# Optimization experiments

Measured on AMD Instinct MI355X. Metric: run time of the kernel, lower is better.

## Reference

```python
import jax, jax.numpy as jnp
import numpy as np

N = 12288          # neuron_count (nodes.shape[0])
R = 1024           # retina_output_size[1]
B = 32             # batch
N_LAYERS = 4       # CONNECTOME_LAYER_NUMBER
DENSITY = 0.05     # adjacency (connectome) sparsity
N_VISUAL = 2048    # neurons flagged 'visual'
N_RATIONAL = 64    # neurons flagged 'rational'


def setup_inputs() -> dict:
    key = jax.random.key(0)
    k_x, k_ret, k_sh, k_adj, k_rat, k_vis, k_ridx = jax.random.split(key, 7)

    x = jax.random.normal(k_x, (B, R), dtype=jnp.float32)

    # Retina layer: Linear(R -> N, bias=False); only rows at visual indices nonzero.
    vis_idx = jax.random.permutation(k_vis, N)[:N_VISUAL]
    vis_mask = jnp.zeros((N,), jnp.float32).at[vis_idx].set(1.0)
    W_retina = jax.random.normal(k_ret, (N, R), dtype=jnp.float32) * vis_mask[:, None]

    # Shared connectome weights: rand(N,N) masked by transposed adjacency != 0.
    adj = jax.random.bernoulli(k_adj, DENSITY, (N, N)).astype(jnp.float32)
    W_shared = jax.random.uniform(k_sh, (N, N), dtype=jnp.float32) * adj

    # Rational layer: Linear(N -> 2); only columns at rational indices nonzero.
    rat_idx = jax.random.permutation(k_ridx, N)[:N_RATIONAL]
    rat_mask = jnp.zeros((N,), jnp.float32).at[rat_idx].set(1.0)
    W_rational = jax.random.normal(k_rat, (2, N), dtype=jnp.float32) * rat_mask[None, :]

    return {"x": x, "W_retina": W_retina, "W_shared": W_shared,
            "W_rational": W_rational, "n_layers": N_LAYERS}


def reference(x, W_retina, W_shared, W_rational, n_layers):
    # retina: out = x @ W_retina^T   -> [B, N]
    out = jnp.einsum('br,nr->bn', x, W_retina)
    # repeated shared-weight Linear (bias-free): out = out @ W_shared^T
    for _ in range(n_layers):
        out = jnp.einsum('bn,mn->bm', out, W_shared)
    # rational readout: [B, 2]
    return jnp.einsum('bn,on->bo', out, W_rational)
```

## Files before the change

### kernel.cpp

```cpp
#include <hip/hip_runtime.h>
#include <cstddef>

#define NN 12288
#define RR 1024
#define BB 32

#define MSEGS 128
#define MROWS (NN / MSEGS)
#define JBLK (NN / 1024)
#define CAP 20

#define PSEGS 256
#define PJ (NN / PSEGS)

typedef float vfloat4 __attribute__((ext_vector_type(4)));

__global__ __launch_bounds__(256) void build_kernel(
    const float* __restrict__ W, float* __restrict__ sval,
    unsigned char* __restrict__ scnt)
{
    const int t   = threadIdx.x;
    const int jb  = blockIdx.x;
    const int seg = blockIdx.y;
    const int j   = jb * 1024 + t * 4;
    const int m0  = seg * MROWS;

    const vfloat4* Wp = (const vfloat4*)(W + (size_t)m0 * NN + j);
    float* v0 = sval + ((size_t)seg * NN + j) * CAP;
    float* v1 = v0 + CAP;
    float* v2 = v0 + 2 * CAP;
    float* v3 = v0 + 3 * CAP;

    int c0 = 0, c1 = 0, c2 = 0, c3 = 0;
    for (int i = 0; i < MROWS; i += 16) {
        vfloat4 w[16];
        #pragma unroll
        for (int u = 0; u < 16; ++u)
            w[u] = __builtin_nontemporal_load(Wp + (size_t)u * (NN / 4));
        Wp += 4 * NN;
        #pragma unroll
        for (int u = 0; u < 16; ++u) {
            const unsigned int li = (unsigned)(i + u);
            if (w[u].x != 0.f) { unsigned int b = __float_as_uint(w[u].x); if (c0 < CAP) v0[c0] = __uint_as_float((b & 0xFFFFFF00u) | li); c0++; }
            if (w[u].y != 0.f) { unsigned int b = __float_as_uint(w[u].y); if (c1 < CAP) v1[c1] = __uint_as_float((b & 0xFFFFFF00u) | li); c1++; }
            if (w[u].z != 0.f) { unsigned int b = __float_as_uint(w[u].z); if (c2 < CAP) v2[c2] = __uint_as_float((b & 0xFFFFFF00u) | li); c2++; }
            if (w[u].w != 0.f) { unsigned int b = __float_as_uint(w[u].w); if (c3 < CAP) v3[c3] = __uint_as_float((b & 0xFFFFFF00u) | li); c3++; }
        }
    }
    uchar4 cn;
    cn.x = (unsigned char)(c0 < CAP ? c0 : CAP);
    cn.y = (unsigned char)(c1 < CAP ? c1 : CAP);
    cn.z = (unsigned char)(c2 < CAP ? c2 : CAP);
    cn.w = (unsigned char)(c3 < CAP ? c3 : CAP);
    *(uchar4*)(scnt + (size_t)seg * NN + j) = cn;
}

__global__ __launch_bounds__(256) void sfold_kernel(
    const float* __restrict__ sval, const unsigned char* __restrict__ scnt,
    const float* __restrict__ hin, float* __restrict__ hpart)
{
    const int seg = blockIdx.y;
    const int j   = blockIdx.x * 256 + threadIdx.x;
    const int m0  = seg * MROWS;

    __shared__ float2 hs[MROWS];
    if (threadIdx.x < MROWS)
        hs[threadIdx.x] = make_float2(hin[m0 + threadIdx.x], hin[NN + m0 + threadIdx.x]);
    __syncthreads();

    const int cnt = scnt[(size_t)seg * NN + j];
    const float4* vp = (const float4*)(sval + ((size_t)seg * NN + j) * CAP);

    float a0 = 0.f, a1 = 0.f;
    const int nq = (cnt + 3) >> 2;
    for (int q = 0; q < nq; ++q) {
        const float4 v4 = vp[q];
        const int k = q * 4;
        #pragma unroll
        for (int u = 0; u < 4; ++u) {
            const float vv = (u == 0) ? v4.x : (u == 1) ? v4.y : (u == 2) ? v4.z : v4.w;
            if (k + u < cnt) {
                const unsigned int b = __float_as_uint(vv);
                const float v = __uint_as_float(b & 0xFFFFFF00u);
                const float2 h = hs[b & 0xFFu];
                a0 = fmaf(v, h.x, a0);
                a1 = fmaf(v, h.y, a1);
            }
        }
    }
    hpart[((size_t)seg * 2) * NN + j]     = a0;
    hpart[((size_t)seg * 2 + 1) * NN + j] = a1;
}

__global__ __launch_bounds__(256) void reduce_h_kernel(
    const float* __restrict__ hpart, float* __restrict__ hout)
{
    const int idx = blockIdx.x * 256 + threadIdx.x;
    float s = 0.f;
    for (int seg = 0; seg < MSEGS; ++seg)
        s += hpart[(size_t)seg * 2 * NN + idx];
    hout[idx] = s;
}

__global__ __launch_bounds__(256) void retina_fold_kernel(
    const float* __restrict__ Wret, const float* __restrict__ h,
    float* __restrict__ ppart)
{
    const int seg = blockIdx.x;
    const int t   = threadIdx.x;
    const int j0  = seg * PJ;

    __shared__ float h0s[PJ];
    __shared__ float h1s[PJ];
    if (t < PJ) {
        h0s[t] = h[j0 + t];
        h1s[t] = h[NN + j0 + t];
    }
    __syncthreads();

    const int r = t * 4;
    float a00 = 0.f, a01 = 0.f, a02 = 0.f, a03 = 0.f;
    float a10 = 0.f, a11 = 0.f, a12 = 0.f, a13 = 0.f;

    const float4* Wp = (const float4*)(Wret + (size_t)j0 * RR + r);
    #pragma unroll 8
    for (int i = 0; i < PJ; ++i) {
        const float4 w = *Wp;
        Wp += RR / 4;
        const float h0 = h0s[i];
        const float h1 = h1s[i];
        a00 = fmaf(h0, w.x, a00); a01 = fmaf(h0, w.y, a01);
        a02 = fmaf(h0, w.z, a02); a03 = fmaf(h0, w.w, a03);
        a10 = fmaf(h1, w.x, a10); a11 = fmaf(h1, w.y, a11);
        a12 = fmaf(h1, w.z, a12); a13 = fmaf(h1, w.w, a13);
    }

    float* d0 = ppart + ((size_t)seg * 2) * RR + r;
    d0[0] = a00; d0[1] = a01; d0[2] = a02; d0[3] = a03;
    float* d1 = d0 + RR;
    d1[0] = a10; d1[1] = a11; d1[2] = a12; d1[3] = a13;
}

__global__ __launch_bounds__(256) void reduce_p_kernel(
    const float* __restrict__ ppart, float* __restrict__ p)
{
    const int idx = blockIdx.x * 256 + threadIdx.x;
    float s = 0.f;
    for (int seg = 0; seg < PSEGS; ++seg)
        s += ppart[(size_t)seg * 2 * RR + idx];
    p[idx] = s;
}

__global__ __launch_bounds__(64) void final_kernel(
    const float* __restrict__ x, const float* __restrict__ p,
    float* __restrict__ out)
{
    const int t = threadIdx.x;
    const int b = t >> 1;
    const int o = t & 1;
    const float4* xp = (const float4*)(x + (size_t)b * RR);
    const float4* pp = (const float4*)(p + (size_t)o * RR);
    float s = 0.f;
    for (int i = 0; i < RR / 4; ++i) {
        const float4 xv = xp[i];
        const float4 pv = pp[i];
        s = fmaf(xv.x, pv.x, s);
        s = fmaf(xv.y, pv.y, s);
        s = fmaf(xv.z, pv.z, s);
        s = fmaf(xv.w, pv.w, s);
    }
    out[b * 2 + o] = s;
}

extern "C" void kernel_launch(void* const* d_in, const int* in_sizes, int n_in,
                              void* d_out, int out_size, void* d_ws, size_t ws_size,
                              hipStream_t stream) {
    const float* x    = (const float*)d_in[0];
    const float* Wret = (const float*)d_in[1];
    const float* Ws   = (const float*)d_in[2];
    const float* Wrat = (const float*)d_in[3];

    char* ws = (char*)d_ws;
    float*         sval  = (float*)(ws + 0);
    unsigned char* scnt  = (unsigned char*)(ws + 125829120);
    float*         hpart = (float*)(ws + 127401984);
    float*         ppart = (float*)(ws + 139984896);
    float*         hA    = (float*)(ws + 142082048);
    float*         hB    = (float*)(ws + 142180352);
    float*         p     = (float*)(ws + 142278656);

    const dim3 buildGrid(JBLK, MSEGS);
    const dim3 sfoldGrid(NN / 256, MSEGS);

    build_kernel<<<buildGrid, 256, 0, stream>>>(Ws, sval, scnt);

    sfold_kernel<<<sfoldGrid, 256, 0, stream>>>(sval, scnt, Wrat, hpart);
    reduce_h_kernel<<<(2 * NN) / 256, 256, 0, stream>>>(hpart, hA);

    sfold_kernel<<<sfoldGrid, 256, 0, stream>>>(sval, scnt, hA, hpart);
    reduce_h_kernel<<<(2 * NN) / 256, 256, 0, stream>>>(hpart, hB);

    sfold_kernel<<<sfoldGrid, 256, 0, stream>>>(sval, scnt, hB, hpart);
    reduce_h_kernel<<<(2 * NN) / 256, 256, 0, stream>>>(hpart, hA);

    sfold_kernel<<<sfoldGrid, 256, 0, stream>>>(sval, scnt, hA, hpart);
    reduce_h_kernel<<<(2 * NN) / 256, 256, 0, stream>>>(hpart, hB);

    retina_fold_kernel<<<PSEGS, 256, 0, stream>>>(Wret, hB, ppart);
    reduce_p_kernel<<<(2 * RR) / 256, 256, 0, stream>>>(ppart, p);

    final_kernel<<<1, 64, 0, stream>>>(x, p, (float*)d_out);
}
```

Baseline: 1.036 ms.

## Stage sparse slots in LDS, transpose layout to slot-major, batch segments in fold

The build kernel now collects nonzeros in shared memory and writes them slot-major (k*NN + j), so each write is a coalesced float4 and only up to the block's maximum count is written. The fold kernel reads the slot-major layout with coalesced per-thread loads and handles four segments per block, which shrinks the partial buffer and the reduction work. The first layer is replaced by a dedicated kernel that reads only the dense W rows at the few nonzero rational indices. The tradeoffs are 80KB of LDS per build block, which limits occupancy, and fold loops whose counts vary between threads, which can cause divergence.

```diff
diff --git a/kernel.cpp b/kernel.cpp
--- a/kernel.cpp
+++ b/kernel.cpp
@@ -9,6 +9,8 @@
 #define MROWS (NN / MSEGS)
 #define JBLK (NN / 1024)
 #define CAP 20
+#define SEGB 4
+#define HSEGS (MSEGS/SEGB)
 
 #define PSEGS 256
 #define PJ (NN / PSEGS)
@@ -19,17 +21,20 @@
     const float* __restrict__ W, float* __restrict__ sval,
     unsigned char* __restrict__ scnt)
 {
+    __shared__ float slots[CAP * 1024];
+    __shared__ int smax;
+
     const int t   = threadIdx.x;
     const int jb  = blockIdx.x;
     const int seg = blockIdx.y;
     const int j   = jb * 1024 + t * 4;
     const int m0  = seg * MROWS;
 
+    if (t == 0) smax = 0;
+    __syncthreads();
+
     const vfloat4* Wp = (const vfloat4*)(W + (size_t)m0 * NN + j);
-    float* v0 = sval + ((size_t)seg * NN + j) * CAP;
-    float* v1 = v0 + CAP;
-    float* v2 = v0 + 2 * CAP;
-    float* v3 = v0 + 3 * CAP;
+    const int base = t * 4;
 
     int c0 = 0, c1 = 0, c2 = 0, c3 = 0;
     for (int i = 0; i < MROWS; i += 16) {
@@ -41,55 +46,99 @@
         #pragma unroll
         for (int u = 0; u < 16; ++u) {
             const unsigned int li = (unsigned)(i + u);
-            if (w[u].x != 0.f) { unsigned int b = __float_as_uint(w[u].x); if (c0 < CAP) v0[c0] = __uint_as_float((b & 0xFFFFFF00u) | li); c0++; }
-            if (w[u].y != 0.f) { unsigned int b = __float_as_uint(w[u].y); if (c1 < CAP) v1[c1] = __uint_as_float((b & 0xFFFFFF00u) | li); c1++; }
-            if (w[u].z != 0.f) { unsigned int b = __float_as_uint(w[u].z); if (c2 < CAP) v2[c2] = __uint_as_float((b & 0xFFFFFF00u) | li); c2++; }
-            if (w[u].w != 0.f) { unsigned int b = __float_as_uint(w[u].w); if (c3 < CAP) v3[c3] = __uint_as_float((b & 0xFFFFFF00u) | li); c3++; }
+            if (w[u].x != 0.f) { unsigned int b = __float_as_uint(w[u].x); if (c0 < CAP) slots[c0 * 1024 + base + 0] = __uint_as_float((b & 0xFFFFFF00u) | li); c0++; }
+            if (w[u].y != 0.f) { unsigned int b = __float_as_uint(w[u].y); if (c1 < CAP) slots[c1 * 1024 + base + 1] = __uint_as_float((b & 0xFFFFFF00u) | li); c1++; }
+            if (w[u].z != 0.f) { unsigned int b = __float_as_uint(w[u].z); if (c2 < CAP) slots[c2 * 1024 + base + 2] = __uint_as_float((b & 0xFFFFFF00u) | li); c2++; }
+            if (w[u].w != 0.f) { unsigned int b = __float_as_uint(w[u].w); if (c3 < CAP) slots[c3 * 1024 + base + 3] = __uint_as_float((b & 0xFFFFFF00u) | li); c3++; }
         }
     }
+    c0 = c0 < CAP ? c0 : CAP;  c1 = c1 < CAP ? c1 : CAP;
+    c2 = c2 < CAP ? c2 : CAP;  c3 = c3 < CAP ? c3 : CAP;
+    int cm = c0 > c1 ? c0 : c1; cm = cm > c2 ? cm : c2; cm = cm > c3 ? cm : c3;
+    atomicMax(&smax, cm);
+    __syncthreads();
+
+    const int kmax = smax;
+    float* dseg = sval + (size_t)seg * CAP * NN + j;
+    for (int k = 0; k < kmax; ++k)
+        *(float4*)(dseg + (size_t)k * NN) = *(const float4*)(slots + k * 1024 + base);
+
     uchar4 cn;
-    cn.x = (unsigned char)(c0 < CAP ? c0 : CAP);
-    cn.y = (unsigned char)(c1 < CAP ? c1 : CAP);
-    cn.z = (unsigned char)(c2 < CAP ? c2 : CAP);
-    cn.w = (unsigned char)(c3 < CAP ? c3 : CAP);
+    cn.x = (unsigned char)c0; cn.y = (unsigned char)c1;
+    cn.z = (unsigned char)c2; cn.w = (unsigned char)c3;
     *(uchar4*)(scnt + (size_t)seg * NN + j) = cn;
+}
+
+__global__ __launch_bounds__(256) void l1_kernel(
+    const float* __restrict__ W, const float* __restrict__ Wrat,
+    float* __restrict__ hout)
+{
+    __shared__ int knt;
+    __shared__ int idxs[128];
+    __shared__ float w0[128], w1[128];
+
+    const int t  = threadIdx.x;
+    const int j  = blockIdx.x * 1024 + t * 4;
+
+    if (t == 0) knt = 0;
+    __syncthreads();
+    for (int m = t; m < NN; m += 256) {
+        const float a = Wrat[m];
+        const float b = Wrat[NN + m];
+        if (a != 0.f || b != 0.f) {
+            const int s = atomicAdd(&knt, 1);
+            idxs[s] = m; w0[s] = a; w1[s] = b;
+        }
+    }
+    __syncthreads();
+    const int K = knt;
+
+    float a00 = 0.f, a01 = 0.f, a02 = 0.f, a03 = 0.f;
+    float a10 = 0.f, a11 = 0.f, a12 = 0.f, a13 = 0.f;
+    for (int k = 0; k < K; ++k) {
+        const float4 wv = *(const float4*)(W + (size_t)idxs[k] * NN + j);
+        const float h0 = w0[k], h1 = w1[k];
+        a00 = fmaf(h0, wv.x, a00); a01 = fmaf(h0, wv.y, a01);
+        a02 = fmaf(h0, wv.z, a02); a03 = fmaf(h0, wv.w, a03);
+        a10 = fmaf(h1, wv.x, a10); a11 = fmaf(h1, wv.y, a11);
+        a12 = fmaf(h1, wv.z, a12); a13 = fmaf(h1, wv.w, a13);
+    }
+    float* d0 = hout + j;
+    d0[0] = a00; d0[1] = a01; d0[2] = a02; d0[3] = a03;
+    float* d1 = hout + NN + j;
+    d1[0] = a10; d1[1] = a11; d1[2] = a12; d1[3] = a13;
 }
 
 __global__ __launch_bounds__(256) void sfold_kernel(
     const float* __restrict__ sval, const unsigned char* __restrict__ scnt,
     const float* __restrict__ hin, float* __restrict__ hpart)
 {
-    const int seg = blockIdx.y;
+    const int sb  = blockIdx.y;
     const int j   = blockIdx.x * 256 + threadIdx.x;
-    const int m0  = seg * MROWS;
-
-    __shared__ float2 hs[MROWS];
-    if (threadIdx.x < MROWS)
-        hs[threadIdx.x] = make_float2(hin[m0 + threadIdx.x], hin[NN + m0 + threadIdx.x]);
-    __syncthreads();
-
-    const int cnt = scnt[(size_t)seg * NN + j];
-    const float4* vp = (const float4*)(sval + ((size_t)seg * NN + j) * CAP);
+    const int m0  = sb * SEGB * MROWS;
+
+    __shared__ float2 hs[SEGB * MROWS];
+    for (int i = threadIdx.x; i < SEGB * MROWS; i += 256)
+        hs[i] = make_float2(hin[m0 + i], hin[NN + m0 + i]);
+    __syncthreads();
 
     float a0 = 0.f, a1 = 0.f;
-    const int nq = (cnt + 3) >> 2;
-    for (int q = 0; q < nq; ++q) {
-        const float4 v4 = vp[q];
-        const int k = q * 4;
-        #pragma unroll
-        for (int u = 0; u < 4; ++u) {
-            const float vv = (u == 0) ? v4.x : (u == 1) ? v4.y : (u == 2) ? v4.z : v4.w;
-            if (k + u < cnt) {
-                const unsigned int b = __float_as_uint(vv);
-                const float v = __uint_as_float(b & 0xFFFFFF00u);
-                const float2 h = hs[b & 0xFFu];
-                a0 = fmaf(v, h.x, a0);
-                a1 = fmaf(v, h.y, a1);
-            }
+    #pragma unroll
+    for (int g = 0; g < SEGB; ++g) {
+        const int seg = sb * SEGB + g;
+        const int cnt = scnt[(size_t)seg * NN + j];
+        const float* vp = sval + (size_t)seg * CAP * NN + j;
+        const float2* hg = hs + g * MROWS;
+        for (int k = 0; k < cnt; ++k) {
+            const unsigned int b = __float_as_uint(vp[(size_t)k * NN]);
+            const float v = __uint_as_float(b & 0xFFFFFF00u);
+            const float2 h = hg[b & 0xFFu];
+            a0 = fmaf(v, h.x, a0);
+            a1 = fmaf(v, h.y, a1);
         }
     }
-    hpart[((size_t)seg * 2) * NN + j]     = a0;
-    hpart[((size_t)seg * 2 + 1) * NN + j] = a1;
+    hpart[((size_t)sb * 2) * NN + j]     = a0;
+    hpart[((size_t)sb * 2 + 1) * NN + j] = a1;
 }
 
 __global__ __launch_bounds__(256) void reduce_h_kernel(
@@ -97,8 +146,8 @@
 {
     const int idx = blockIdx.x * 256 + threadIdx.x;
     float s = 0.f;
-    for (int seg = 0; seg < MSEGS; ++seg)
-        s += hpart[(size_t)seg * 2 * NN + idx];
+    for (int sb = 0; sb < HSEGS; ++sb)
+        s += hpart[(size_t)sb * 2 * NN + idx];
     hout[idx] = s;
 }
 
@@ -184,18 +233,17 @@
     float*         sval  = (float*)(ws + 0);
     unsigned char* scnt  = (unsigned char*)(ws + 125829120);
     float*         hpart = (float*)(ws + 127401984);
-    float*         ppart = (float*)(ws + 139984896);
-    float*         hA    = (float*)(ws + 142082048);
-    float*         hB    = (float*)(ws + 142180352);
-    float*         p     = (float*)(ws + 142278656);
+    float*         ppart = (float*)(ws + 130547712);
+    float*         hA    = (float*)(ws + 132644864);
+    float*         hB    = (float*)(ws + 132743168);
+    float*         p     = (float*)(ws + 132841472);
 
     const dim3 buildGrid(JBLK, MSEGS);
-    const dim3 sfoldGrid(NN / 256, MSEGS);
+    const dim3 sfoldGrid(NN / 256, HSEGS);
 
     build_kernel<<<buildGrid, 256, 0, stream>>>(Ws, sval, scnt);
 
-    sfold_kernel<<<sfoldGrid, 256, 0, stream>>>(sval, scnt, Wrat, hpart);
-    reduce_h_kernel<<<(2 * NN) / 256, 256, 0, stream>>>(hpart, hA);
+    l1_kernel<<<JBLK, 256, 0, stream>>>(Ws, Wrat, hA);
 
     sfold_kernel<<<sfoldGrid, 256, 0, stream>>>(sval, scnt, hA, hpart);
     reduce_h_kernel<<<(2 * NN) / 256, 256, 0, stream>>>(hpart, hB);
```

New measurement: 938.3 us. 9.5% less time.
